# Optimization experiments

Hardware: AMD Instinct MI355X
Metric: run time of the kernel (lower is better)

## Reference

```python
import jax, jax.numpy as jnp
import numpy as np

N_SAT = 1536
N_UAV = 1536
D = 64


def setup_inputs() -> dict:
    key = jax.random.key(0)
    ks = jax.random.split(key, 8)
    sat_regions = jax.random.normal(ks[0], (N_SAT, D), dtype=jnp.float32)
    uav_regions = jax.random.normal(ks[1], (N_UAV, D), dtype=jnp.float32)
    # weights in [in, out] layout (transpose of torch Linear), scaled like kaiming-ish init
    W1 = jax.random.normal(ks[2], (2 * D, D), dtype=jnp.float32) / np.sqrt(2 * D)
    b1 = jnp.zeros((D,), dtype=jnp.float32)
    W2 = jax.random.normal(ks[3], (D, D // 2), dtype=jnp.float32) / np.sqrt(D)
    b2 = jnp.zeros((D // 2,), dtype=jnp.float32)
    W3 = jax.random.normal(ks[4], (D // 2, 1), dtype=jnp.float32) / np.sqrt(D // 2)
    b3 = jnp.zeros((1,), dtype=jnp.float32)
    return {"sat_regions": sat_regions, "uav_regions": uav_regions,
            "W1": W1, "b1": b1, "W2": W2, "b2": b2, "W3": W3, "b3": b3}


def reference(sat_regions, uav_regions, W1, b1, W2, b2, W3, b3):
    d = sat_regions.shape[-1]
    # Layer 1 on concat([sat, uav]) == sat @ W1[:d] + uav @ W1[d:], broadcast over pairs.
    h_sat = sat_regions @ W1[:d]            # [N, D]
    h_uav = uav_regions @ W1[d:]            # [M, D]
    h1 = jax.nn.relu(h_sat[:, None, :] + h_uav[None, :, :] + b1)   # [N, M, D]
    h2 = jax.nn.relu(h1 @ W2 + b2)                                  # [N, M, D/2]
    sim = jax.nn.sigmoid((h2 @ W3 + b3)[..., 0])                    # [N, M]

    # Greedy bipartite assignment: for each sat row in order, pick best unused uav.
    def step(mask, row):
        scores = jnp.where(mask, row, jnp.float32(-1.0))  # used entries set to -1, as in torch
        j = jnp.argmax(scores)
        return mask.at[j].set(False), j

    mask0 = jnp.ones((sim.shape[1],), dtype=bool)
    _, assign = jax.lax.scan(step, mask0, sim)            # assign: [N] int32
    matched_uav = uav_regions[assign]                      # [N, D]
    # aligned_pairs as a stacked array: [N, 2, D] = (sat_i, uav_{assign[i]})
    return jnp.stack([sat_regions, matched_uav], axis=1)
```

## Files before the change

### kernel.cpp

```cpp
#include <hip/hip_runtime.h>
#include <float.h>

#define NS 1536
#define DD 64

static const size_t OFF_A  = 0;
static const size_t OFF_C2 = 98304;
static const size_t OFF_L  = 196608;
static const size_t OFF_AS = 196608 + (size_t)NS * NS;

__global__ __launch_bounds__(64) void kA(const float* __restrict__ sat,
                                         const float* __restrict__ uav,
                                         const float* __restrict__ W1,
                                         const float* __restrict__ b1,
                                         float* __restrict__ A,
                                         float* __restrict__ C2) {
    const int row = blockIdx.x;
    const int d = threadIdx.x;
    float accA = b1[d];
    float accC = 0.f;
    const float* __restrict__ satr = sat + row * DD;
    const float* __restrict__ uavr = uav + row * DD;
#pragma unroll 8
    for (int k = 0; k < DD; ++k) {
        accA = fmaf(satr[k], W1[k * DD + d], accA);
        accC = fmaf(uavr[k], W1[(DD + k) * DD + d], accC);
    }
    A[row * DD + d] = accA;
    C2[((size_t)(d >> 2) * NS + row) * 4 + (d & 3)] = accC;
}

__global__ __launch_bounds__(256) void kB(const float* __restrict__ A,
                                          const float* __restrict__ C2,
                                          const float* __restrict__ W2,
                                          const float* __restrict__ b2,
                                          const float* __restrict__ W3,
                                          float* __restrict__ L) {
    const int lane = threadIdx.x & 63;
    const int wave = threadIdx.x >> 6;
    const int i = __builtin_amdgcn_readfirstlane(blockIdx.x * 4 + wave);
    const int jbase = blockIdx.y * 256;
    const float* __restrict__ Ar = A + (size_t)i * DD;

    float u[4][32];
#pragma unroll
    for (int o = 0; o < 32; ++o) {
        const float b = b2[o];
        u[0][o] = b; u[1][o] = b; u[2][o] = b; u[3][o] = b;
    }

    const float4* __restrict__ C2v = (const float4*)C2;

    for (int d4 = 0; d4 < 16; ++d4) {
        float c[4][4];
#pragma unroll
        for (int p = 0; p < 4; ++p) {
            const float4 t = C2v[(size_t)d4 * NS + jbase + p * 64 + lane];
            c[p][0] = t.x; c[p][1] = t.y; c[p][2] = t.z; c[p][3] = t.w;
        }
#pragma unroll
        for (int dd = 0; dd < 4; ++dd) {
            const float a = Ar[d4 * 4 + dd];
            const float v0 = fmaxf(a + c[0][dd], 0.f);
            const float v1 = fmaxf(a + c[1][dd], 0.f);
            const float v2 = fmaxf(a + c[2][dd], 0.f);
            const float v3 = fmaxf(a + c[3][dd], 0.f);
            const float* __restrict__ w2r = W2 + (d4 * 4 + dd) * 32;
#pragma unroll
            for (int o = 0; o < 32; ++o) {
                const float w = w2r[o];
                u[0][o] = fmaf(v0, w, u[0][o]);
                u[1][o] = fmaf(v1, w, u[1][o]);
                u[2][o] = fmaf(v2, w, u[2][o]);
                u[3][o] = fmaf(v3, w, u[3][o]);
            }
        }
    }

#pragma unroll
    for (int p = 0; p < 4; ++p) {
        float acc = 0.f;
#pragma unroll
        for (int o = 0; o < 32; ++o)
            acc = fmaf(fmaxf(u[p][o], 0.f), W3[o], acc);
        L[(size_t)i * NS + jbase + p * 64 + lane] = acc;
    }
}

__global__ __launch_bounds__(256) void kC(const float* __restrict__ L,
                                          unsigned short* __restrict__ top) {
    __shared__ int hist[256];
    __shared__ int suff[256];
    __shared__ float cv[1024];
    __shared__ int ci[1024];
    __shared__ int s_cnt, s_B0, s_base, s_B1;
    const int t = threadIdx.x;
    const int row = blockIdx.x;
    const float* __restrict__ Lr = L + (size_t)row * NS;

    top[row * 256 + t] = 0xFFFFu;

    hist[t] = 0;
    if (t == 0) s_cnt = 0;
    __syncthreads();

    unsigned ub[6]; float fv[6];
#pragma unroll
    for (int k = 0; k < 6; ++k) {
        const float x = Lr[t + 256 * k];
        fv[k] = x;
        unsigned b = __float_as_uint(x);
        b = (b & 0x80000000u) ? ~b : (b | 0x80000000u);
        ub[k] = b;
        atomicAdd(&hist[b >> 24], 1);
    }
    __syncthreads();

    suff[t] = hist[t];
    __syncthreads();
    for (int off = 1; off < 256; off <<= 1) {
        const int v = (t + off < 256) ? suff[t + off] : 0;
        __syncthreads();
        suff[t] += v;
        __syncthreads();
    }
    if (suff[t] >= 256 && (t == 255 || suff[t + 1] < 256)) {
        s_B0 = t;
        s_base = (t == 255) ? 0 : suff[t + 1];
    }
    __syncthreads();
    const unsigned B0 = (unsigned)s_B0;
    const int base = s_base;

    hist[t] = 0;
    __syncthreads();
#pragma unroll
    for (int k = 0; k < 6; ++k)
        if ((ub[k] >> 24) == B0) atomicAdd(&hist[(ub[k] >> 16) & 255], 1);
    __syncthreads();
    suff[t] = hist[t];
    __syncthreads();
    for (int off = 1; off < 256; off <<= 1) {
        const int v = (t + off < 256) ? suff[t + off] : 0;
        __syncthreads();
        suff[t] += v;
        __syncthreads();
    }
    const int need = 256 - base;
    if (suff[t] >= need && (t == 255 || suff[t + 1] < need)) s_B1 = t;
    __syncthreads();
    const unsigned B1 = (unsigned)s_B1;
    const int m = base + suff[B1];
    if (m > 1024) return;

#pragma unroll
    for (int k = 0; k < 6; ++k) {
        const unsigned hi = ub[k] >> 24;
        const unsigned mid = (ub[k] >> 16) & 255u;
        if (hi > B0 || (hi == B0 && mid >= B1)) {
            const int pos = atomicAdd(&s_cnt, 1);
            cv[pos] = fv[k];
            ci[pos] = t + 256 * k;
        }
    }
    __syncthreads();

    for (int e = t; e < m; e += 256) {
        const float v = cv[e]; const int id = ci[e];
        int r = 0;
        for (int s2 = 0; s2 < m; ++s2) {
            const float vs = cv[s2];
            if (vs > v || (vs == v && ci[s2] < id)) ++r;
        }
        if (r < 256) top[row * 256 + (r & 63) * 4 + (r >> 6)] = (unsigned short)id;
    }
}

__device__ __forceinline__ unsigned wave_max_u32_dpp(unsigned x) {
    unsigned t;
    t = (unsigned)__builtin_amdgcn_update_dpp(0, (int)x, 0x111, 0xF, 0xF, true);
    x = x > t ? x : t;
    t = (unsigned)__builtin_amdgcn_update_dpp(0, (int)x, 0x112, 0xF, 0xF, true);
    x = x > t ? x : t;
    t = (unsigned)__builtin_amdgcn_update_dpp(0, (int)x, 0x114, 0xF, 0xF, true);
    x = x > t ? x : t;
    t = (unsigned)__builtin_amdgcn_update_dpp(0, (int)x, 0x118, 0xF, 0xF, true);
    x = x > t ? x : t;
    t = (unsigned)__builtin_amdgcn_update_dpp(0, (int)x, 0x142, 0xF, 0xF, true);
    x = x > t ? x : t;
    t = (unsigned)__builtin_amdgcn_update_dpp(0, (int)x, 0x143, 0xF, 0xF, true);
    x = x > t ? x : t;
    return x;
}

__global__ __launch_bounds__(64) void kD(const float* __restrict__ L,
                                         const unsigned short* __restrict__ top,
                                         int* __restrict__ assign) {
    __shared__ int used_s[NS];
    __shared__ int assign_s[NS];
    __shared__ unsigned short U_s[NS];
    const int lane = threadIdx.x;
    for (int k = lane; k < NS; k += 64) used_s[k] = 0;
    __syncthreads();

    const uint2* __restrict__ T = (const uint2*)top;

    uint2 buf[16];
#pragma unroll
    for (int k = 0; k < 16; ++k) buf[k] = T[k * 64 + lane];

    int f0 = 0, f1 = 0, f2 = 0, f3 = 0;
    int jprev = -1;
    int mU = NS;

    for (int g = 0; g < NS; g += 8) {
        if ((g & 63) == 0) {
            int fl[24];
#pragma unroll
            for (int k = 0; k < 24; ++k) fl[k] = used_s[lane + (k << 6)];
            int cnt = 0;
#pragma unroll
            for (int k = 0; k < 24; ++k) cnt += (fl[k] == 0);
            int incl = cnt;
#pragma unroll
            for (int o = 1; o < 64; o <<= 1) {
                const int v = __shfl_up(incl, o);
                if (lane >= o) incl += v;
            }
            int pos = incl - cnt;
#pragma unroll
            for (int k = 0; k < 24; ++k) {
                if (fl[k] == 0) { U_s[pos] = (unsigned short)(lane + (k << 6)); ++pos; }
            }
            mU = __builtin_amdgcn_readlane(incl, 63);
        }

        uint2 nb[8];
#pragma unroll
        for (int k = 0; k < 8; ++k) {
            int r = g + 16 + k;
            r = (r < NS) ? r : (NS - 1);
            nb[k] = T[r * 64 + lane];
        }

#pragma unroll
        for (int q = 0; q < 8; ++q) {
            const int i = g + q;

            const uint2 pn = buf[q + 1];
            const int n0 = (int)(pn.x & 0xFFFFu), n1 = (int)(pn.x >> 16);
            const int n2 = (int)(pn.y & 0xFFFFu), n3 = (int)(pn.y >> 16);
            const int g0 = used_s[n0 < NS ? n0 : 0];
            const int g1 = used_s[n1 < NS ? n1 : 0];
            const int g2 = used_s[n2 < NS ? n2 : 0];
            const int g3 = used_s[n3 < NS ? n3 : 0];

            const uint2 pc = buf[q];
            const int c0 = (int)(pc.x & 0xFFFFu), c1 = (int)(pc.x >> 16);
            const int c2 = (int)(pc.y & 0xFFFFu), c3 = (int)(pc.y >> 16);
            const bool a0 = (c0 < NS) && (f0 == 0) && (c0 != jprev);
            const bool a1 = (c1 < NS) && (f1 == 0) && (c1 != jprev);
            const bool a2 = (c2 < NS) && (f2 == 0) && (c2 != jprev);
            const bool a3 = (c3 < NS) && (f3 == 0) && (c3 != jprev);
            const unsigned long long b0 = __ballot(a0);
            const unsigned long long b1 = __ballot(a1);
            const unsigned long long b2 = __ballot(a2);
            const unsigned long long b3 = __ballot(a3);

            int j;
            if (b0)      j = __builtin_amdgcn_readlane(c0, __ffsll(b0) - 1);
            else if (b1) j = __builtin_amdgcn_readlane(c1, __ffsll(b1) - 1);
            else if (b2) j = __builtin_amdgcn_readlane(c2, __ffsll(b2) - 1);
            else if (b3) j = __builtin_amdgcn_readlane(c3, __ffsll(b3) - 1);
            else {
                const float* __restrict__ Lr = L + (size_t)i * NS;
                float bv = -FLT_MAX; int bi = NS;
                for (int kbase = 0; kbase < mU; kbase += 512) {
                    int idx[8]; int flc[8]; float vv[8];
#pragma unroll
                    for (int c = 0; c < 8; ++c) {
                        const int k = kbase + lane + (c << 6);
                        idx[c] = (k < mU) ? (int)U_s[k] : 0;
                    }
#pragma unroll
                    for (int c = 0; c < 8; ++c) flc[c] = used_s[idx[c]];
#pragma unroll
                    for (int c = 0; c < 8; ++c) vv[c] = Lr[idx[c]];
#pragma unroll
                    for (int c = 0; c < 8; ++c) {
                        const int k = kbase + lane + (c << 6);
                        if (k < mU && flc[c] == 0 &&
                            (vv[c] > bv || (vv[c] == bv && idx[c] < bi))) {
                            bv = vv[c]; bi = idx[c];
                        }
                    }
                }
                unsigned key = __float_as_uint(bv);
                key = (key & 0x80000000u) ? ~key : (key | 0x80000000u);
                const unsigned wk = wave_max_u32_dpp(key);
                const unsigned maxk =
                    (unsigned)__builtin_amdgcn_readlane((int)wk, 63);
                unsigned cand = (key == maxk) ? (unsigned)(NS - bi) : 0u;
                const unsigned wc = wave_max_u32_dpp(cand);
                const unsigned mc =
                    (unsigned)__builtin_amdgcn_readlane((int)wc, 63);
                j = NS - (int)mc;
            }
            if (lane == 0) { used_s[j] = 1; assign_s[i] = j; }
            jprev = j;
            f0 = g0; f1 = g1; f2 = g2; f3 = g3;
        }

#pragma unroll
        for (int k = 0; k < 8; ++k) buf[k] = buf[k + 8];
#pragma unroll
        for (int k = 0; k < 8; ++k) buf[k + 8] = nb[k];
    }

    for (int k = lane; k < NS; k += 64) assign[k] = assign_s[k];
}

__global__ __launch_bounds__(128) void kE(const float* __restrict__ sat,
                                          const float* __restrict__ uav,
                                          const int* __restrict__ assign,
                                          float* __restrict__ out) {
    const int i = blockIdx.x;
    const int t = threadIdx.x;
    if (t < 64) out[(size_t)i * 128 + t] = sat[(size_t)i * DD + t];
    else        out[(size_t)i * 128 + t] = uav[(size_t)assign[i] * DD + (t - 64)];
}

extern "C" void kernel_launch(void* const* d_in, const int* in_sizes, int n_in,
                              void* d_out, int out_size, void* d_ws, size_t ws_size,
                              hipStream_t stream) {
    const float* sat = (const float*)d_in[0];
    const float* uav = (const float*)d_in[1];
    const float* W1  = (const float*)d_in[2];
    const float* b1  = (const float*)d_in[3];
    const float* W2  = (const float*)d_in[4];
    const float* b2  = (const float*)d_in[5];
    const float* W3  = (const float*)d_in[6];

    float* ws = (float*)d_ws;
    float* A   = ws + OFF_A;
    float* C2  = ws + OFF_C2;
    float* L   = ws + OFF_L;
    int* assign = (int*)(ws + OFF_AS);
    unsigned short* top = (unsigned short*)(ws + OFF_A);

    hipLaunchKernelGGL(kA, dim3(NS), dim3(64), 0, stream, sat, uav, W1, b1, A, C2);
    hipLaunchKernelGGL(kB, dim3(NS / 4, NS / 256), dim3(256), 0, stream,
                       A, C2, W2, b2, W3, L);
    hipLaunchKernelGGL(kC, dim3(NS), dim3(256), 0, stream, L, top);
    hipLaunchKernelGGL(kD, dim3(1), dim3(64), 0, stream, L, top, assign);
    hipLaunchKernelGGL(kE, dim3(NS), dim3(128), 0, stream, sat, uav, assign,
                       (float*)d_out);
}
```

Baseline: 871.9 us.

## Prefetch L rows two steps ahead for predicted fallback scans in greedy assignment

In the serial greedy-assignment kernel, the code now predicts two rows ahead whether all of a row's top-candidate list is already used. When it is, that row of L is loaded into registers early, along with a snapshot of a new bitmask of used columns. When the fallback is then needed, it scans the register copy instead of issuing dependent global loads, with the column picked one step earlier excluded via jprev. This hides global-memory latency on the serial critical path. The cost is extra registers, some speculative loads that go unused, and a second used-column bitmask to keep in sync.

```diff
diff --git a/kernel.cpp b/kernel.cpp
--- a/kernel.cpp
+++ b/kernel.cpp
@@ -199,8 +199,10 @@
     __shared__ int used_s[NS];
     __shared__ int assign_s[NS];
     __shared__ unsigned short U_s[NS];
+    __shared__ unsigned used_b[NS / 32];
     const int lane = threadIdx.x;
     for (int k = lane; k < NS; k += 64) used_s[k] = 0;
+    if (lane < NS / 32) used_b[lane] = 0u;
     __syncthreads();
 
     const uint2* __restrict__ T = (const uint2*)top;
@@ -212,6 +214,10 @@
     int f0 = 0, f1 = 0, f2 = 0, f3 = 0;
     int jprev = -1;
     int mU = NS;
+
+    float4   rv[2][6];
+    unsigned mw[2][6];
+    int      svalid[2] = {0, 0};
 
     for (int g = 0; g < NS; g += 8) {
         if ((g & 63) == 0) {
@@ -246,6 +252,7 @@
 #pragma unroll
         for (int q = 0; q < 8; ++q) {
             const int i = g + q;
+            const int pq = q & 1;
 
             const uint2 pn = buf[q + 1];
             const int n0 = (int)(pn.x & 0xFFFFu), n1 = (int)(pn.x >> 16);
@@ -254,6 +261,14 @@
             const int g1 = used_s[n1 < NS ? n1 : 0];
             const int g2 = used_s[n2 < NS ? n2 : 0];
             const int g3 = used_s[n3 < NS ? n3 : 0];
+
+            const uint2 ph = buf[q + 2];
+            const int h0 = (int)(ph.x & 0xFFFFu), h1 = (int)(ph.x >> 16);
+            const int h2 = (int)(ph.y & 0xFFFFu), h3 = (int)(ph.y >> 16);
+            const int u0 = used_s[h0 < NS ? h0 : 0];
+            const int u1 = used_s[h1 < NS ? h1 : 0];
+            const int u2 = used_s[h2 < NS ? h2 : 0];
+            const int u3 = used_s[h3 < NS ? h3 : 0];
 
             const uint2 pc = buf[q];
             const int c0 = (int)(pc.x & 0xFFFFu), c1 = (int)(pc.x >> 16);
@@ -272,6 +287,37 @@
             else if (b1) j = __builtin_amdgcn_readlane(c1, __ffsll(b1) - 1);
             else if (b2) j = __builtin_amdgcn_readlane(c2, __ffsll(b2) - 1);
             else if (b3) j = __builtin_amdgcn_readlane(c3, __ffsll(b3) - 1);
+            else if (svalid[pq]) {
+                float bv = -FLT_MAX; int bi = NS;
+                const int bsh = 4 * (lane & 7);
+#pragma unroll
+                for (int m = 0; m < 6; ++m) {
+                    const float4 v4 = rv[pq][m];
+                    const unsigned w = mw[pq][m];
+                    const int colb = 4 * lane + 256 * m;
+                    const float vs[4] = {v4.x, v4.y, v4.z, v4.w};
+#pragma unroll
+                    for (int sub = 0; sub < 4; ++sub) {
+                        const int col = colb + sub;
+                        const bool free_ = (((w >> (bsh + sub)) & 1u) == 0u) &&
+                                           (col != jprev);
+                        const float v = vs[sub];
+                        if (free_ && (v > bv || (v == bv && col < bi))) {
+                            bv = v; bi = col;
+                        }
+                    }
+                }
+                unsigned key = __float_as_uint(bv);
+                key = (key & 0x80000000u) ? ~key : (key | 0x80000000u);
+                const unsigned wk = wave_max_u32_dpp(key);
+                const unsigned maxk =
+                    (unsigned)__builtin_amdgcn_readlane((int)wk, 63);
+                unsigned cand = (key == maxk) ? (unsigned)(NS - bi) : 0u;
+                const unsigned wc = wave_max_u32_dpp(cand);
+                const unsigned mc =
+                    (unsigned)__builtin_amdgcn_readlane((int)wc, 63);
+                j = NS - (int)mc;
+            }
             else {
                 const float* __restrict__ Lr = L + (size_t)i * NS;
                 float bv = -FLT_MAX; int bi = NS;
@@ -306,9 +352,33 @@
                     (unsigned)__builtin_amdgcn_readlane((int)wc, 63);
                 j = NS - (int)mc;
             }
-            if (lane == 0) { used_s[j] = 1; assign_s[i] = j; }
+            if (lane == 0) {
+                used_s[j] = 1;
+                used_b[j >> 5] |= (1u << (j & 31));
+                assign_s[i] = j;
+            }
             jprev = j;
             f0 = g0; f1 = g1; f2 = g2; f3 = g3;
+
+            {
+                const bool hfree =
+                    (h0 < NS && u0 == 0) || (h1 < NS && u1 == 0) ||
+                    (h2 < NS && u2 == 0) || (h3 < NS && u3 == 0);
+                const unsigned long long hball = __ballot(hfree);
+                int pv = 0;
+                if (hball == 0ULL && (i + 2) < NS) {
+                    pv = 1;
+                    const float4* __restrict__ Lr2 =
+                        (const float4*)(L + (size_t)(i + 2) * NS);
+#pragma unroll
+                    for (int m = 0; m < 6; ++m)
+                        rv[pq][m] = Lr2[lane + 64 * m];
+#pragma unroll
+                    for (int m = 0; m < 6; ++m)
+                        mw[pq][m] = used_b[(lane >> 3) + 8 * m];
+                }
+                svalid[pq] = pv;
+            }
         }
 
 #pragma unroll
```

After: 1.274 ms. 46.2% more time.
